# Performance work log

Measured on AMD Instinct MI355X. Metric: run time of the kernel, lower is better.

## Reference

```python
import jax, jax.numpy as jnp
import numpy as np

B, T, D, L = 8, 8192, 256, 3
DISTS = (1, 5, 15, 30)


def _layernorm(x, g, b, eps=1e-5):
    m = x.mean(-1, keepdims=True)
    v = ((x - m) ** 2).mean(-1, keepdims=True)
    return (x - m) * jax.lax.rsqrt(v + eps) * g + b


def _temporal_edges():
    src, dst = [], []
    for d in DISTS:
        a = np.arange(T - d)
        src += [a, a + d]
        dst += [a + d, a]
    ei = np.stack([np.concatenate(src), np.concatenate(dst)])  # [2, E]
    off = (np.arange(B) * T).repeat(ei.shape[1])
    return np.tile(ei, (1, B)) + off[None, :]  # [2, B*E]


def setup_inputs() -> dict:
    key = jax.random.key(0)
    ks = jax.random.split(key, 6)
    s = 1.0 / np.sqrt(D)
    s4 = 1.0 / np.sqrt(4 * D)
    return dict(
        x=jax.random.normal(ks[0], (B, T, D), jnp.float32),
        adjacency=jnp.zeros((T, T), jnp.float32),  # shape-check only
        edge_index=jnp.asarray(_temporal_edges(), jnp.int32),
        conv_w=jax.random.normal(ks[1], (L, D, D), jnp.float32) * s,
        conv_b=jnp.zeros((L, D), jnp.float32),
        norm_g=jnp.ones((L, D), jnp.float32),
        norm_b=jnp.zeros((L, D), jnp.float32),
        normff_g=jnp.ones((D,), jnp.float32),
        normff_b=jnp.zeros((D,), jnp.float32),
        w1=jax.random.normal(ks[2], (D, 4 * D), jnp.float32) * s,
        b1=jnp.zeros((4 * D,), jnp.float32),
        w2=jax.random.normal(ks[3], (4 * D, D), jnp.float32) * s4,
        b2=jnp.zeros((D,), jnp.float32),
    )


def reference(x, adjacency, edge_index, conv_w, conv_b, norm_g, norm_b,
              normff_g, normff_b, w1, b1, w2, b2):
    b, t, d = x.shape
    n = b * t
    xf = x.reshape(n, d)
    src, dst = edge_index[0], edge_index[1]
    # GCN symmetric degree normalization (no self loops), degrees by target node
    deg = jax.ops.segment_sum(jnp.ones(src.shape[0], x.dtype), dst, num_segments=n)
    dinv = jnp.where(deg > 0, jax.lax.rsqrt(deg), 0.0)
    enorm = (dinv[src] * dinv[dst])[:, None]  # [E,1]
    for i in range(conv_w.shape[0]):
        h = xf @ conv_w[i]                                    # [N,D]
        h = jax.ops.segment_sum(h[src] * enorm, dst, num_segments=n) + conv_b[i]
        h = jax.nn.gelu(h, approximate=False)
        h = _layernorm(h.reshape(b, t, d), norm_g[i], norm_b[i]).reshape(n, d)
        xf = xf + h
    x = xf.reshape(b, t, d)
    y = _layernorm(x, normff_g, normff_b)
    ff = jax.nn.gelu(y @ w1 + b1, approximate=False) @ w2 + b2
    return x + ff
```

## Files before the change

kernel.cpp:

```cpp
#include <hip/hip_runtime.h>
#include <hip/hip_bf16.h>
#include <math.h>
#include <stdint.h>
#include <stddef.h>

#define TB 8
#define TT 8192
#define DD 256
#define NR (TB * TT)
#define HH 1024
#define LL 3

typedef unsigned short ushort_t;
typedef __attribute__((ext_vector_type(8))) short short8;
typedef __attribute__((ext_vector_type(4))) float floatx4;

__device__ __forceinline__ float bf2f(ushort_t u) {
  union { unsigned int i; float f; } x; x.i = ((unsigned int)u) << 16; return x.f;
}
__device__ __forceinline__ ushort_t f2bf(float f) {
  union { float f; unsigned int i; } x; x.f = f;
  unsigned int r = x.i + 0x7fffu + ((x.i >> 16) & 1u);
  return (ushort_t)(r >> 16);
}
__device__ __forceinline__ float ld_in(const void* p, size_t i, int isf) {
  return isf ? ((const float*)p)[i] : bf2f(((const ushort_t*)p)[i]);
}
__device__ __forceinline__ float gelu_f(float v) {
  const float y = v * (0.7978845608028654f + 0.035677408136300125f * v * v);
  const float e = __expf(-2.0f * y);
  return v * __builtin_amdgcn_rcpf(1.0f + e);
}
__device__ __forceinline__ int deg_of(int t) {
  return (t >= 1) + (t >= 5) + (t >= 15) + (t >= 30)
       + (t < TT - 1) + (t < TT - 5) + (t < TT - 15) + (t < TT - 30);
}
__device__ __forceinline__ void gl_lds16(const ushort_t* g, void* l) {
  __builtin_amdgcn_global_load_lds(
      (const __attribute__((address_space(1))) unsigned int*)(g),
      (__attribute__((address_space(3))) unsigned int*)(l), 16, 0, 0);
}
__device__ __forceinline__ int xcd_swz(int lin, int nwg) {
  const int q = nwg >> 3;
  return (lin & 7) * q + (lin >> 3);
}
__device__ __forceinline__ int swz128(int row, int bytecol) {
  return row * 128 + (bytecol ^ ((row & 7) << 4));
}
__device__ __forceinline__ int swz64(int row, int bytecol) {
  return row * 64 + (bytecol ^ ((row & 3) << 4));
}
#define WAIT_VM0()  asm volatile("s_waitcnt vmcnt(0)" ::: "memory")
#define WAIT_LGKM0() asm volatile("s_waitcnt lgkmcnt(0)" ::: "memory")

__global__ void k_probe(const void* __restrict__ x, int* __restrict__ flag) {
  if (threadIdx.x == 0 && blockIdx.x == 0) {
    const float* fb = (const float*)x;
    int okf = 0;
    for (int i = 0; i < 128; ++i) {
      const float av = fabsf(fb[i]);
      if (av > 1e-6f && av < 100.f) okf++;
    }
    *flag = (okf >= 115) ? 1 : 0;
  }
}

__global__ __launch_bounds__(256) void k_cvt(const void* __restrict__ x,
                                             ushort_t* __restrict__ xb,
                                             const int* __restrict__ flag) {
  const int isf = *flag;
  const size_t i4 = (size_t)blockIdx.x * 256 + threadIdx.x;
  if (isf) {
    const float4 f = ((const float4*)x)[i4];
    ushort4 u; u.x = f2bf(f.x); u.y = f2bf(f.y); u.z = f2bf(f.z); u.w = f2bf(f.w);
    ((ushort4*)xb)[i4] = u;
  } else {
    ((ushort4*)xb)[i4] = ((const ushort4*)x)[i4];
  }
}

__global__ void k_transpose_all(const void* __restrict__ cw,
                                const void* __restrict__ w1,
                                const void* __restrict__ w2,
                                ushort_t* __restrict__ cwT,
                                ushort_t* __restrict__ w1T,
                                ushort_t* __restrict__ w2T,
                                const int* __restrict__ flag) {
  __shared__ ushort_t tile[32][33];
  const int isf = *flag;
  const int b = blockIdx.x;
  const void* src; ushort_t* dst; int R, C, bx, by; size_t row0;
  if (b < 192) {
    const int i = b >> 6, t = b & 63;
    src = cw; dst = cwT + (size_t)i * DD * DD; row0 = (size_t)i * DD;
    R = DD; C = DD; bx = (t & 7) * 32; by = (t >> 3) * 32;
  } else if (b < 448) {
    const int t = b - 192;
    src = w1; dst = w1T; row0 = 0; R = DD; C = HH;
    bx = (t & 31) * 32; by = (t >> 5) * 32;
  } else {
    const int t = b - 448;
    src = w2; dst = w2T; row0 = 0; R = HH; C = DD;
    bx = (t & 7) * 32; by = (t >> 3) * 32;
  }
  const int tx = threadIdx.x;
  for (int i = threadIdx.y; i < 32; i += 8)
    tile[i][tx] = f2bf(ld_in(src, (row0 + by + i) * (size_t)C + bx + tx, isf));
  __syncthreads();
  for (int i = threadIdx.y; i < 32; i += 8)
    dst[(size_t)(bx + i) * R + by + tx] = tile[tx][i];
}

__global__ __launch_bounds__(256, 2) void k_conv_fused(
    const ushort_t* __restrict__ xin, ushort_t* __restrict__ xout,
    const ushort_t* __restrict__ Bt, const void* __restrict__ bias,
    size_t boff, const void* __restrict__ g, const void* __restrict__ bn,
    size_t goff, const int* __restrict__ flag) {
  __shared__ alignas(16) char smem[68096];
  float* scr    = (float*)smem;
  float* part   = scr;
  float* partsq = scr + 256;
  float* smu    = scr + 512;
  float* srs    = scr + 576;
  char* aggA    = smem + 2560;
  char* rt      = smem + 2560;
  const int isf = *flag;

  const int tid  = threadIdx.x;
  const int lane = tid & 63;
  const int l16  = lane & 15;
  const int quad = lane >> 4;
  const int w    = tid >> 6;
  const int m0   = xcd_swz(blockIdx.x, gridDim.x) * 64;

  char* lB = smem + 35328 + w * 8192;

  const int srow = lane >> 3;
  const int sseg = (lane & 7) ^ (srow & 7);
  auto stageB = [&](int kc) {
#pragma unroll
    for (int i = 0; i < 8; ++i)
      gl_lds16(Bt + (size_t)(w * 64 + i * 8 + srow) * DD + kc * 64 + sseg * 8,
               lB + i * 1024);
  };
  stageB(0);

  const int tbase = m0 & (TT - 1);
  const bool interior = (tbase >= 60) && (tbase <= TT - 124);
  const int koffs[8] = {-30, -15, -5, -1, 1, 5, 15, 30};
#pragma unroll
  for (int j = 0; j < 8; ++j) {
    const int id = j * 256 + tid;
    const int r = id >> 5, c = id & 31;
    const ushort_t* base = xin + (size_t)(m0 + r) * DD + c * 8;
    float s[8] = {0.f, 0.f, 0.f, 0.f, 0.f, 0.f, 0.f, 0.f};
    if (interior) {
#pragma unroll
      for (int e = 0; e < 8; ++e) {
        const short8 u = *(const short8*)(base + (ptrdiff_t)koffs[e] * DD);
#pragma unroll
        for (int q2 = 0; q2 < 8; ++q2) s[q2] += bf2f((ushort_t)u[q2]);
      }
#pragma unroll
      for (int q2 = 0; q2 < 8; ++q2) s[q2] *= 0.125f;
    } else {
      const int t = tbase + r;
      const float di = rsqrtf((float)deg_of(t));
#pragma unroll
      for (int e = 0; e < 8; ++e) {
        const int t2 = t + koffs[e];
        if ((unsigned)t2 < (unsigned)TT) {
          const float wgt = di * rsqrtf((float)deg_of(t2));
          const short8 u = *(const short8*)(base + (ptrdiff_t)koffs[e] * DD);
#pragma unroll
          for (int q2 = 0; q2 < 8; ++q2) s[q2] += wgt * bf2f((ushort_t)u[q2]);
        }
      }
    }
    short8 o;
#pragma unroll
    for (int q2 = 0; q2 < 8; ++q2) o[q2] = (short)f2bf(s[q2]);
    *(short8*)(aggA + (c >> 3) * 8192 + swz128(r, (c & 7) * 16)) = o;
  }
  WAIT_LGKM0();
  __builtin_amdgcn_s_barrier();
  __builtin_amdgcn_sched_barrier(0);

  floatx4 acc[4][4];
#pragma unroll
  for (int i = 0; i < 4; ++i)
#pragma unroll
    for (int j = 0; j < 4; ++j) acc[i][j] = {0.f, 0.f, 0.f, 0.f};

#pragma unroll
  for (int kc = 0; kc < 4; ++kc) {
    WAIT_VM0();
    short8 af0[4], bf0[4], af1[4], bf1[4];
#pragma unroll
    for (int mt = 0; mt < 4; ++mt) {
      af0[mt] = *(const short8*)(aggA + kc * 8192 +
                   swz128(mt * 16 + l16, quad * 16));
      af1[mt] = *(const short8*)(aggA + kc * 8192 +
                   swz128(mt * 16 + l16, 64 + quad * 16));
    }
#pragma unroll
    for (int nt = 0; nt < 4; ++nt) {
      bf0[nt] = *(const short8*)(lB + swz128(nt * 16 + l16, quad * 16));
      bf1[nt] = *(const short8*)(lB + swz128(nt * 16 + l16, 64 + quad * 16));
    }
    WAIT_LGKM0();
    __builtin_amdgcn_sched_barrier(0);
    if (kc < 3) stageB(kc + 1);
#pragma unroll
    for (int mt = 0; mt < 4; ++mt)
#pragma unroll
      for (int nt = 0; nt < 4; ++nt)
        acc[mt][nt] = __builtin_amdgcn_mfma_f32_16x16x32_bf16(
            af0[mt], bf0[nt], acc[mt][nt], 0, 0, 0);
#pragma unroll
    for (int mt = 0; mt < 4; ++mt)
#pragma unroll
      for (int nt = 0; nt < 4; ++nt)
        acc[mt][nt] = __builtin_amdgcn_mfma_f32_16x16x32_bf16(
            af1[mt], bf1[nt], acc[mt][nt], 0, 0, 0);
  }

#pragma unroll
  for (int nt = 0; nt < 4; ++nt) {
    const float bv = ld_in(bias, boff + w * 64 + nt * 16 + l16, isf);
#pragma unroll
    for (int mt = 0; mt < 4; ++mt)
#pragma unroll
      for (int r = 0; r < 4; ++r)
        acc[mt][nt][r] = gelu_f(acc[mt][nt][r] + bv);
  }
#pragma unroll
  for (int mt = 0; mt < 4; ++mt) {
#pragma unroll
    for (int r = 0; r < 4; ++r) {
      float p = 0.f, q = 0.f;
#pragma unroll
      for (int nt = 0; nt < 4; ++nt) {
        const float v = acc[mt][nt][r];
        p += v; q += v * v;
      }
#pragma unroll
      for (int o = 8; o > 0; o >>= 1) {
        p += __shfl_xor(p, o, 64);
        q += __shfl_xor(q, o, 64);
      }
      if (l16 == 0) {
        const int rowloc = mt * 16 + quad * 4 + r;
        part[w * 64 + rowloc] = p;
        partsq[w * 64 + rowloc] = q;
      }
    }
  }
  __syncthreads();
  if (tid < 64) {
    const float s  = part[tid] + part[64 + tid] + part[128 + tid] + part[192 + tid];
    const float sq = partsq[tid] + partsq[64 + tid] + partsq[128 + tid] + partsq[192 + tid];
    const float mu = s * (1.0f / DD);
    const float var = sq * (1.0f / DD) - mu * mu;
    smu[tid] = mu;
    srs[tid] = rsqrtf(var + 1e-5f);
  }
  __syncthreads();

#pragma unroll
  for (int nt = 0; nt < 4; ++nt) {
    const int col = w * 64 + nt * 16 + l16;
    const float gv = ld_in(g, goff + col, isf);
    const float bnv = ld_in(bn, goff + col, isf);
#pragma unroll
    for (int mt = 0; mt < 4; ++mt) {
#pragma unroll
      for (int r = 0; r < 4; ++r) {
        const int rowloc = mt * 16 + quad * 4 + r;
        *(ushort_t*)(rt + (rowloc * 264 + col) * 2) =
            f2bf((acc[mt][nt][r] - smu[rowloc]) * srs[rowloc] * gv + bnv);
      }
    }
  }
  __syncthreads();

#pragma unroll
  for (int i = 0; i < 8; ++i) {
    const int ch = tid + i * 256;
    const int row = ch >> 5, sg = ch & 31;
    const short8 xv = *(const short8*)(xin + (size_t)(m0 + row) * DD + sg * 8);
    const short8 rv = *(const short8*)(rt + (row * 264 + sg * 8) * 2);
    short8 ov;
#pragma unroll
    for (int j = 0; j < 8; ++j)
      ov[j] = (short)f2bf(bf2f((ushort_t)xv[j]) + bf2f((ushort_t)rv[j]));
    *(short8*)(xout + (size_t)(m0 + row) * DD + sg * 8) = ov;
  }
}

__global__ __launch_bounds__(256, 2) void k_ffn(
    const ushort_t* __restrict__ xb, const ushort_t* __restrict__ w1T,
    const ushort_t* __restrict__ w2T, const void* __restrict__ gff,
    const void* __restrict__ bff, const void* __restrict__ b1,
    const void* __restrict__ b2, void* __restrict__ dout,
    const int* __restrict__ flag) {
  __shared__ alignas(16) char smem[65536];
  char* An = smem;
  char* Zs = smem + 32768;
  char* Rs = smem;
  const int isf = *flag;

  const int tid  = threadIdx.x;
  const int lane = tid & 63;
  const int l16  = lane & 15;
  const int quad = lane >> 4;
  const int w    = tid >> 6;
  const int m0   = xcd_swz(blockIdx.x, gridDim.x) * 64;
  char* Bw = smem + 49152 + w * 4096;

  const int sr8 = lane >> 3;
  const int ss8 = (lane & 7) ^ (sr8 & 7);
  auto stageB1 = [&](int n1, int kc) {
#pragma unroll
    for (int i = 0; i < 4; ++i)
      gl_lds16(w1T + (size_t)(n1 * 128 + w * 32 + i * 8 + sr8) * DD +
                   kc * 64 + ss8 * 8,
               Bw + i * 1024);
  };
  const int sr4 = lane >> 2;
  const int ss4 = (lane & 3) ^ (sr4 & 3);
  auto stageB2 = [&](int n1, int kc2, int ks) {
#pragma unroll
    for (int i = 0; i < 4; ++i)
      gl_lds16(w2T + (size_t)(w * 64 + i * 16 + sr4) * HH +
                   n1 * 128 + kc2 * 64 + ks * 32 + ss4 * 8,
               Bw + i * 1024);
  };

  stageB1(0, 0);

  const int sg = tid & 31;
  float gffv[8], bffv[8];
#pragma unroll
  for (int j = 0; j < 8; ++j) {
    gffv[j] = ld_in(gff, sg * 8 + j, isf);
    bffv[j] = ld_in(bff, sg * 8 + j, isf);
  }
#pragma unroll
  for (int i = 0; i < 8; ++i) {
    const int row = (tid + i * 256) >> 5;
    const short8 xv = *(const short8*)(xb + (size_t)(m0 + row) * DD + sg * 8);
    float v[8], ps = 0.f, pq = 0.f;
#pragma unroll
    for (int j = 0; j < 8; ++j) {
      v[j] = bf2f((ushort_t)xv[j]); ps += v[j]; pq += v[j] * v[j];
    }
#pragma unroll
    for (int o = 16; o > 0; o >>= 1) {
      ps += __shfl_xor(ps, o, 64);
      pq += __shfl_xor(pq, o, 64);
    }
    const float mu = ps * (1.0f / DD);
    const float rs = rsqrtf(pq * (1.0f / DD) - mu * mu + 1e-5f);
    short8 o8;
#pragma unroll
    for (int j = 0; j < 8; ++j)
      o8[j] = (short)f2bf((v[j] - mu) * rs * gffv[j] + bffv[j]);
    *(short8*)(An + (sg >> 3) * 8192 + swz128(row, (sg & 7) * 16)) = o8;
  }
  WAIT_LGKM0();
  __builtin_amdgcn_s_barrier();
  __builtin_amdgcn_sched_barrier(0);

  floatx4 acc2[4][4];
#pragma unroll
  for (int i = 0; i < 4; ++i)
#pragma unroll
    for (int j = 0; j < 4; ++j) acc2[i][j] = {0.f, 0.f, 0.f, 0.f};

  for (int n1 = 0; n1 < 8; ++n1) {
    floatx4 acc1[4][2];
#pragma unroll
    for (int i = 0; i < 4; ++i)
#pragma unroll
      for (int j = 0; j < 2; ++j) acc1[i][j] = {0.f, 0.f, 0.f, 0.f};

#pragma unroll
    for (int kc = 0; kc < 4; ++kc) {
      WAIT_VM0();
      short8 af0[4], af1[4], bq0[2], bq1[2];
#pragma unroll
      for (int mt = 0; mt < 4; ++mt)
        af0[mt] = *(const short8*)(An + kc * 8192 +
                     swz128(mt * 16 + l16, quad * 16));
#pragma unroll
      for (int nt = 0; nt < 2; ++nt)
        bq0[nt] = *(const short8*)(Bw + swz128(nt * 16 + l16, quad * 16));
#pragma unroll
      for (int mt = 0; mt < 4; ++mt)
#pragma unroll
        for (int nt = 0; nt < 2; ++nt)
          acc1[mt][nt] = __builtin_amdgcn_mfma_f32_16x16x32_bf16(
              af0[mt], bq0[nt], acc1[mt][nt], 0, 0, 0);
#pragma unroll
      for (int mt = 0; mt < 4; ++mt)
        af1[mt] = *(const short8*)(An + kc * 8192 +
                     swz128(mt * 16 + l16, 64 + quad * 16));
#pragma unroll
      for (int nt = 0; nt < 2; ++nt)
        bq1[nt] = *(const short8*)(Bw + swz128(nt * 16 + l16, 64 + quad * 16));
      WAIT_LGKM0();
      __builtin_amdgcn_sched_barrier(0);
      if (kc < 3) stageB1(n1, kc + 1);
#pragma unroll
      for (int mt = 0; mt < 4; ++mt)
#pragma unroll
        for (int nt = 0; nt < 2; ++nt)
          acc1[mt][nt] = __builtin_amdgcn_mfma_f32_16x16x32_bf16(
              af1[mt], bq1[nt], acc1[mt][nt], 0, 0, 0);
    }

#pragma unroll
    for (int nt = 0; nt < 2; ++nt) {
      const int col = w * 32 + nt * 16 + l16;
      const float b1v = ld_in(b1, n1 * 128 + col, isf);
#pragma unroll
      for (int mt = 0; mt < 4; ++mt)
#pragma unroll
        for (int r = 0; r < 4; ++r) {
          const int row = mt * 16 + quad * 4 + r;
          *(ushort_t*)(Zs + (col >> 6) * 8192 + swz128(row, (col & 63) * 2)) =
              f2bf(gelu_f(acc1[mt][nt][r] + b1v));
        }
    }
    stageB2(n1, 0, 0);
    WAIT_LGKM0();
    __builtin_amdgcn_s_barrier();
    __builtin_amdgcn_sched_barrier(0);

#pragma unroll
    for (int kc2 = 0; kc2 < 2; ++kc2) {
#pragma unroll
      for (int ks = 0; ks < 2; ++ks) {
        WAIT_VM0();
        short8 af[4], bfr[4];
#pragma unroll
        for (int mt = 0; mt < 4; ++mt)
          af[mt] = *(const short8*)(Zs + kc2 * 8192 +
                     swz128(mt * 16 + l16, ks * 64 + quad * 16));
#pragma unroll
        for (int nt = 0; nt < 4; ++nt)
          bfr[nt] = *(const short8*)(Bw + swz64(nt * 16 + l16, quad * 16));
        WAIT_LGKM0();
        __builtin_amdgcn_sched_barrier(0);
        if (kc2 == 0 || ks == 0) stageB2(n1, kc2 + (ks & 1), (ks + 1) & 1);
        else if (n1 < 7) stageB1(n1 + 1, 0);
#pragma unroll
        for (int mt = 0; mt < 4; ++mt)
#pragma unroll
          for (int nt = 0; nt < 4; ++nt)
            acc2[mt][nt] = __builtin_amdgcn_mfma_f32_16x16x32_bf16(
                af[mt], bfr[nt], acc2[mt][nt], 0, 0, 0);
      }
    }
    __builtin_amdgcn_s_barrier();
    __builtin_amdgcn_sched_barrier(0);
  }

  WAIT_VM0();
#pragma unroll
  for (int i = 0; i < 8; ++i)
    gl_lds16(xb + (size_t)(m0 + ((i * 256 + tid) >> 5)) * DD +
                 ((i * 256 + tid) & 31) * 8,
             Rs + i * 4096 + w * 1024);
  __syncthreads();

#pragma unroll
  for (int nt = 0; nt < 4; ++nt) {
    const int col = w * 64 + nt * 16 + l16;
    const float b2v = ld_in(b2, col, isf);
#pragma unroll
    for (int mt = 0; mt < 4; ++mt) {
#pragma unroll
      for (int r = 0; r < 4; ++r) {
        const int lr = mt * 16 + quad * 4 + r;
        const float v = acc2[mt][nt][r] + b2v +
                        bf2f(*(const ushort_t*)(Rs + lr * 512 + col * 2));
        const size_t idx = (size_t)(m0 + lr) * DD + col;
        if (isf) ((float*)dout)[idx] = v;
        else     ((ushort_t*)dout)[idx] = f2bf(v);
      }
    }
  }
}

extern "C" void kernel_launch(void* const* d_in, const int* in_sizes, int n_in,
                              void* d_out, int out_size, void* d_ws, size_t ws_size,
                              hipStream_t stream) {
  const void* x      = d_in[0];
  const void* conv_w = d_in[3];
  const void* conv_b = d_in[4];
  const void* norm_g = d_in[5];
  const void* norm_b = d_in[6];
  const void* nff_g  = d_in[7];
  const void* nff_b  = d_in[8];
  const void* w1     = d_in[9];
  const void* b1     = d_in[10];
  const void* w2     = d_in[11];
  const void* b2     = d_in[12];
  (void)in_sizes; (void)n_in; (void)out_size; (void)ws_size;

  char* ws = (char*)d_ws;
  int*      flag = (int*)ws;      ws += 16;
  ushort_t* xA   = (ushort_t*)ws; ws += (size_t)NR * DD * 2;
  ushort_t* xB   = (ushort_t*)ws; ws += (size_t)NR * DD * 2;
  ushort_t* cwT  = (ushort_t*)ws; ws += (size_t)LL * DD * DD * 2;
  ushort_t* w1T  = (ushort_t*)ws; ws += (size_t)DD * HH * 2;
  ushort_t* w2T  = (ushort_t*)ws; ws += (size_t)HH * DD * 2;

  k_probe<<<1, 64, 0, stream>>>(x, flag);
  k_transpose_all<<<704, dim3(32, 8), 0, stream>>>(
      conv_w, w1, w2, cwT, w1T, w2T, flag);
  k_cvt<<<(NR * DD / 4) / 256, 256, 0, stream>>>(x, xA, flag);

  k_conv_fused<<<NR / 64, 256, 0, stream>>>(
      xA, xB, cwT, conv_b, 0, norm_g, norm_b, 0, flag);
  k_conv_fused<<<NR / 64, 256, 0, stream>>>(
      xB, xA, cwT + (size_t)DD * DD, conv_b, DD, norm_g, norm_b, DD, flag);
  k_conv_fused<<<NR / 64, 256, 0, stream>>>(
      xA, xB, cwT + (size_t)2 * DD * DD, conv_b, 2 * DD, norm_g, norm_b,
      2 * DD, flag);

  k_ffn<<<NR / 64, 256, 0, stream>>>(
      xB, w1T, w2T, nff_g, nff_b, b1, b2, d_out, flag);
}
```

Measured before the change: 640.6 us.

## Merge all phases into one cooperative persistent kernel with grid syncs

Replaces the separate transpose, convert, three conv and FFN launches with a single cooperative kernel of 512 blocks. Each block handles two row tiles per phase, and grid-wide syncs separate the phases, removing inter-kernel launch gaps and tail effects. If the cooperative launch fails, the code falls back to per-phase kernels that also use the two-tiles-per-block split. The risks are the cost of grid sync, lower occupancy (512 blocks at 2 per CU), and extra __syncthreads per tile.

```diff
diff --git a/kernel.cpp b/kernel.cpp
--- a/kernel.cpp
+++ b/kernel.cpp
@@ -1,8 +1,11 @@
 #include <hip/hip_runtime.h>
+#include <hip/hip_cooperative_groups.h>
 #include <hip/hip_bf16.h>
 #include <math.h>
 #include <stdint.h>
 #include <stddef.h>
+
+namespace cg = cooperative_groups;
 
 #define TB 8
 #define TT 8192
@@ -65,30 +68,10 @@
   }
 }
 
-__global__ __launch_bounds__(256) void k_cvt(const void* __restrict__ x,
-                                             ushort_t* __restrict__ xb,
-                                             const int* __restrict__ flag) {
-  const int isf = *flag;
-  const size_t i4 = (size_t)blockIdx.x * 256 + threadIdx.x;
-  if (isf) {
-    const float4 f = ((const float4*)x)[i4];
-    ushort4 u; u.x = f2bf(f.x); u.y = f2bf(f.y); u.z = f2bf(f.z); u.w = f2bf(f.w);
-    ((ushort4*)xb)[i4] = u;
-  } else {
-    ((ushort4*)xb)[i4] = ((const ushort4*)x)[i4];
-  }
-}
-
-__global__ void k_transpose_all(const void* __restrict__ cw,
-                                const void* __restrict__ w1,
-                                const void* __restrict__ w2,
-                                ushort_t* __restrict__ cwT,
-                                ushort_t* __restrict__ w1T,
-                                ushort_t* __restrict__ w2T,
-                                const int* __restrict__ flag) {
-  __shared__ ushort_t tile[32][33];
-  const int isf = *flag;
-  const int b = blockIdx.x;
+__device__ __forceinline__ void transpose_tile(
+    char* smem_, const void* cw, const void* w1, const void* w2,
+    ushort_t* cwT, ushort_t* w1T, ushort_t* w2T, int isf, int b, int tid) {
+  ushort_t (*tile)[33] = (ushort_t(*)[33])smem_;
   const void* src; ushort_t* dst; int R, C, bx, by; size_t row0;
   if (b < 192) {
     const int i = b >> 6, t = b & 63;
@@ -103,20 +86,44 @@
     src = w2; dst = w2T; row0 = 0; R = HH; C = DD;
     bx = (t & 7) * 32; by = (t >> 3) * 32;
   }
-  const int tx = threadIdx.x;
-  for (int i = threadIdx.y; i < 32; i += 8)
+  const int tx = tid & 31, ty = tid >> 5;
+  __syncthreads();
+  for (int i = ty; i < 32; i += 8)
     tile[i][tx] = f2bf(ld_in(src, (row0 + by + i) * (size_t)C + bx + tx, isf));
   __syncthreads();
-  for (int i = threadIdx.y; i < 32; i += 8)
+  for (int i = ty; i < 32; i += 8)
     dst[(size_t)(bx + i) * R + by + tx] = tile[tx][i];
 }
 
-__global__ __launch_bounds__(256, 2) void k_conv_fused(
-    const ushort_t* __restrict__ xin, ushort_t* __restrict__ xout,
+__device__ __forceinline__ void phase0(
+    char* smem, const void* x, ushort_t* xA, const void* cw,
+    const void* w1, const void* w2, ushort_t* cwT, ushort_t* w1T,
+    ushort_t* w2T, int isf, int bid, int tid) {
+  transpose_tile(smem, cw, w1, w2, cwT, w1T, w2T, isf, bid, tid);
+  if (bid < 192)
+    transpose_tile(smem, cw, w1, w2, cwT, w1T, w2T, isf, 512 + bid, tid);
+  const size_t c0 = (size_t)bid * 8192 + tid;
+  if (isf) {
+    const float4* xf = (const float4*)x;
+    ushort4* xo = (ushort4*)xA;
+#pragma unroll
+    for (int i = 0; i < 32; ++i) {
+      const float4 f = xf[c0 + i * 256];
+      ushort4 u; u.x = f2bf(f.x); u.y = f2bf(f.y); u.z = f2bf(f.z); u.w = f2bf(f.w);
+      xo[c0 + i * 256] = u;
+    }
+  } else {
+#pragma unroll
+    for (int i = 0; i < 32; ++i)
+      ((ushort4*)xA)[c0 + i * 256] = ((const ushort4*)x)[c0 + i * 256];
+  }
+}
+
+__device__ __forceinline__ void conv_tile(
+    char* smem, const ushort_t* __restrict__ xin, ushort_t* __restrict__ xout,
     const ushort_t* __restrict__ Bt, const void* __restrict__ bias,
     size_t boff, const void* __restrict__ g, const void* __restrict__ bn,
-    size_t goff, const int* __restrict__ flag) {
-  __shared__ alignas(16) char smem[68096];
+    size_t goff, int isf, int m0, int tid) {
   float* scr    = (float*)smem;
   float* part   = scr;
   float* partsq = scr + 256;
@@ -124,16 +131,14 @@
   float* srs    = scr + 576;
   char* aggA    = smem + 2560;
   char* rt      = smem + 2560;
-  const int isf = *flag;
-
-  const int tid  = threadIdx.x;
+
   const int lane = tid & 63;
   const int l16  = lane & 15;
   const int quad = lane >> 4;
   const int w    = tid >> 6;
-  const int m0   = xcd_swz(blockIdx.x, gridDim.x) * 64;
-
   char* lB = smem + 35328 + w * 8192;
+
+  __syncthreads();
 
   const int srow = lane >> 3;
   const int sseg = (lane & 7) ^ (srow & 7);
@@ -298,25 +303,23 @@
   }
 }
 
-__global__ __launch_bounds__(256, 2) void k_ffn(
-    const ushort_t* __restrict__ xb, const ushort_t* __restrict__ w1T,
-    const ushort_t* __restrict__ w2T, const void* __restrict__ gff,
-    const void* __restrict__ bff, const void* __restrict__ b1,
-    const void* __restrict__ b2, void* __restrict__ dout,
-    const int* __restrict__ flag) {
-  __shared__ alignas(16) char smem[65536];
+__device__ __forceinline__ void ffn_tile(
+    char* smem, const ushort_t* __restrict__ xb,
+    const ushort_t* __restrict__ w1T, const ushort_t* __restrict__ w2T,
+    const void* __restrict__ gff, const void* __restrict__ bff,
+    const void* __restrict__ b1, const void* __restrict__ b2,
+    void* __restrict__ dout, int isf, int m0, int tid) {
   char* An = smem;
   char* Zs = smem + 32768;
   char* Rs = smem;
-  const int isf = *flag;
-
-  const int tid  = threadIdx.x;
+
   const int lane = tid & 63;
   const int l16  = lane & 15;
   const int quad = lane >> 4;
   const int w    = tid >> 6;
-  const int m0   = xcd_swz(blockIdx.x, gridDim.x) * 64;
   char* Bw = smem + 49152 + w * 4096;
+
+  __syncthreads();
 
   const int sr8 = lane >> 3;
   const int ss8 = (lane & 7) ^ (sr8 & 7);
@@ -492,6 +495,70 @@
       }
     }
   }
+}
+
+__global__ __launch_bounds__(256, 2) void k_mega(
+    const void* x, ushort_t* xA, ushort_t* xB,
+    const void* cw, const void* w1, const void* w2,
+    ushort_t* cwT, ushort_t* w1T, ushort_t* w2T,
+    const void* conv_b, const void* norm_g, const void* norm_b,
+    const void* gff, const void* bff, const void* b1, const void* b2,
+    void* dout, const int* flag) {
+  cg::grid_group gg = cg::this_grid();
+  __shared__ alignas(16) char smem[68096];
+  const int isf = *flag;
+  const int tid = threadIdx.x;
+  const int bid = blockIdx.x;
+  const int t0 = xcd_swz(bid, 512);
+
+  phase0(smem, x, xA, cw, w1, w2, cwT, w1T, w2T, isf, bid, tid);
+  __threadfence();
+  gg.sync();
+
+  for (int l = 0; l < LL; ++l) {
+    const ushort_t* xin = (l == 1) ? xB : xA;
+    ushort_t* xout = (l == 1) ? xA : xB;
+    const ushort_t* Bt = cwT + (size_t)l * DD * DD;
+    conv_tile(smem, xin, xout, Bt, conv_b, (size_t)l * DD, norm_g, norm_b,
+              (size_t)l * DD, isf, t0 * 64, tid);
+    conv_tile(smem, xin, xout, Bt, conv_b, (size_t)l * DD, norm_g, norm_b,
+              (size_t)l * DD, isf, (t0 + 512) * 64, tid);
+    __threadfence();
+    gg.sync();
+  }
+
+  ffn_tile(smem, xB, w1T, w2T, gff, bff, b1, b2, dout, isf, t0 * 64, tid);
+  ffn_tile(smem, xB, w1T, w2T, gff, bff, b1, b2, dout, isf, (t0 + 512) * 64, tid);
+}
+
+__global__ __launch_bounds__(256, 2) void k_phase0(
+    const void* x, ushort_t* xA, const void* cw, const void* w1,
+    const void* w2, ushort_t* cwT, ushort_t* w1T, ushort_t* w2T,
+    const int* flag) {
+  __shared__ alignas(16) char smem[68096];
+  phase0(smem, x, xA, cw, w1, w2, cwT, w1T, w2T, *flag, blockIdx.x, threadIdx.x);
+}
+__global__ __launch_bounds__(256, 2) void k_conv2(
+    const ushort_t* xin, ushort_t* xout, const ushort_t* Bt,
+    const void* bias, size_t boff, const void* g, const void* bn,
+    size_t goff, const int* flag) {
+  __shared__ alignas(16) char smem[68096];
+  const int t0 = xcd_swz(blockIdx.x, 512);
+  conv_tile(smem, xin, xout, Bt, bias, boff, g, bn, goff, *flag,
+            t0 * 64, threadIdx.x);
+  conv_tile(smem, xin, xout, Bt, bias, boff, g, bn, goff, *flag,
+            (t0 + 512) * 64, threadIdx.x);
+}
+__global__ __launch_bounds__(256, 2) void k_ffn2(
+    const ushort_t* xb, const ushort_t* w1T, const ushort_t* w2T,
+    const void* gff, const void* bff, const void* b1, const void* b2,
+    void* dout, const int* flag) {
+  __shared__ alignas(16) char smem[68096];
+  const int t0 = xcd_swz(blockIdx.x, 512);
+  ffn_tile(smem, xb, w1T, w2T, gff, bff, b1, b2, dout, *flag,
+           t0 * 64, threadIdx.x);
+  ffn_tile(smem, xb, w1T, w2T, gff, bff, b1, b2, dout, *flag,
+           (t0 + 512) * 64, threadIdx.x);
 }
 
 extern "C" void kernel_launch(void* const* d_in, const int* in_sizes, int n_in,
@@ -519,18 +586,28 @@
   ushort_t* w2T  = (ushort_t*)ws; ws += (size_t)HH * DD * 2;
 
   k_probe<<<1, 64, 0, stream>>>(x, flag);
-  k_transpose_all<<<704, dim3(32, 8), 0, stream>>>(
-      conv_w, w1, w2, cwT, w1T, w2T, flag);
-  k_cvt<<<(NR * DD / 4) / 256, 256, 0, stream>>>(x, xA, flag);
-
-  k_conv_fused<<<NR / 64, 256, 0, stream>>>(
-      xA, xB, cwT, conv_b, 0, norm_g, norm_b, 0, flag);
-  k_conv_fused<<<NR / 64, 256, 0, stream>>>(
-      xB, xA, cwT + (size_t)DD * DD, conv_b, DD, norm_g, norm_b, DD, flag);
-  k_conv_fused<<<NR / 64, 256, 0, stream>>>(
-      xA, xB, cwT + (size_t)2 * DD * DD, conv_b, 2 * DD, norm_g, norm_b,
-      2 * DD, flag);
-
-  k_ffn<<<NR / 64, 256, 0, stream>>>(
-      xB, w1T, w2T, nff_g, nff_b, b1, b2, d_out, flag);
-}
+
+  void* kargs[] = {
+      (void*)&x, (void*)&xA, (void*)&xB,
+      (void*)&conv_w, (void*)&w1, (void*)&w2,
+      (void*)&cwT, (void*)&w1T, (void*)&w2T,
+      (void*)&conv_b, (void*)&norm_g, (void*)&norm_b,
+      (void*)&nff_g, (void*)&nff_b, (void*)&b1, (void*)&b2,
+      (void*)&d_out, (void*)&flag};
+  const hipError_t e = hipLaunchCooperativeKernel(
+      (const void*)k_mega, dim3(512), dim3(256), kargs, 0, stream);
+  if (e != hipSuccess) {
+    (void)hipGetLastError();
+    k_phase0<<<512, 256, 0, stream>>>(x, xA, conv_w, w1, w2, cwT, w1T, w2T,
+                                      flag);
+    for (int l = 0; l < LL; ++l) {
+      const ushort_t* xin = (l == 1) ? xB : xA;
+      ushort_t* xout = (l == 1) ? xA : xB;
+      k_conv2<<<512, 256, 0, stream>>>(
+          xin, xout, cwT + (size_t)l * DD * DD, conv_b, (size_t)l * DD,
+          norm_g, norm_b, (size_t)l * DD, flag);
+    }
+    k_ffn2<<<512, 256, 0, stream>>>(xB, w1T, w2T, nff_g, nff_b, b1, b2,
+                                    d_out, flag);
+  }
+}
```

Result: slower. 1.362 ms (+112.6%).
